# Optimization experiments

Hardware: AMD Instinct MI355X
Metric: run time of the kernel (lower is better)

## Reference

```python
import jax, jax.numpy as jnp
import numpy as np

N_EMBED = 1024
N_HEAD = 16
HEAD_DIM = N_EMBED // N_HEAD


def setup_inputs() -> dict:
    key = jax.random.key(0)
    k1, k2, k3, k4, k5 = jax.random.split(key, 5)
    x = jax.random.normal(k1, (4, 2048, N_EMBED), dtype=jnp.float32)
    s = 1.0 / np.sqrt(N_EMBED)
    W_attn = jax.random.normal(k2, (N_EMBED, 3 * N_EMBED), dtype=jnp.float32) * s
    b_attn = jnp.zeros((3 * N_EMBED,), dtype=jnp.float32)
    W_proj = jax.random.normal(k3, (N_EMBED, N_EMBED), dtype=jnp.float32) * s
    b_proj = jnp.zeros((N_EMBED,), dtype=jnp.float32)
    return {"x": x, "W_attn": W_attn, "b_attn": b_attn, "W_proj": W_proj, "b_proj": b_proj}


def reference(x, W_attn, b_attn, W_proj, b_proj):
    B, T, C = x.shape
    qkv = x @ W_attn + b_attn  # [B, T, 3C]
    q, k, v = jnp.split(qkv, 3, axis=2)
    # [B, H, T, D]
    q = q.reshape(B, T, N_HEAD, HEAD_DIM).transpose(0, 2, 1, 3)
    k = k.reshape(B, T, N_HEAD, HEAD_DIM).transpose(0, 2, 1, 3)
    v = v.reshape(B, T, N_HEAD, HEAD_DIM).transpose(0, 2, 1, 3)
    scale = 1.0 / np.sqrt(HEAD_DIM)
    scores = jnp.einsum('bhqd,bhkd->bhqk', q, k) * scale
    causal = jnp.tril(jnp.ones((T, T), dtype=bool))
    scores = jnp.where(causal[None, None], scores, -jnp.inf)
    attn = jax.nn.softmax(scores, axis=-1)
    y = jnp.einsum('bhqk,bhkd->bhqd', attn, v)
    y = y.transpose(0, 2, 1, 3).reshape(B, T, C)
    return y @ W_proj + b_proj
```

## Files before the change

kernel.cpp:

```cpp
#include <hip/hip_runtime.h>

typedef unsigned short u16;
typedef unsigned int u32;
typedef unsigned long long u64;
typedef __attribute__((ext_vector_type(8))) __bf16 b8;
typedef __attribute__((ext_vector_type(4))) float f32x4;

#define T_SEQ 2048
#define NB 4
#define NH 16
#define HD 64
#define CEMB 1024
#define M_ROWS (NB * T_SEQ)
#define Q_PRESCALE 0.18033688011112042f

__device__ __forceinline__ u16 f2bf(float f) {
  union { float f; unsigned int u; } v; v.f = f;
  unsigned int r = v.u + 0x7FFFu + ((v.u >> 16) & 1u);
  return (u16)(r >> 16);
}

__device__ __forceinline__ u32 pk2bf(float a, float b) {
  __bf16 x = (__bf16)a, y = (__bf16)b;
  return (u32)*(u16*)&x | ((u32)*(u16*)&y << 16);
}

__device__ __forceinline__ void gl_lds16(const u16* g, u16* l) {
  __builtin_amdgcn_global_load_lds(
      (const __attribute__((address_space(1))) unsigned int*)g,
      (__attribute__((address_space(3))) unsigned int*)l, 16, 0, 0);
}

#define BARRIER() __builtin_amdgcn_s_barrier()
#define LGKM0() do { asm volatile("s_waitcnt lgkmcnt(0)" ::: "memory"); \
                     __builtin_amdgcn_sched_barrier(0); } while (0)
#define VMCNT4() asm volatile("s_waitcnt vmcnt(4)" ::: "memory")
#define VMCNT2() asm volatile("s_waitcnt vmcnt(2)" ::: "memory")
#define VMCNT0() asm volatile("s_waitcnt vmcnt(0)" ::: "memory")

__global__ void k_convert(const float* __restrict__ in, u16* __restrict__ out, int n4) {
  int i = blockIdx.x * blockDim.x + threadIdx.x;
  int stride = gridDim.x * blockDim.x;
  for (; i < n4; i += stride) {
    float4 v = ((const float4*)in)[i];
    ushort4 o;
    o.x = f2bf(v.x); o.y = f2bf(v.y); o.z = f2bf(v.z); o.w = f2bf(v.w);
    ((ushort4*)out)[i] = o;
  }
}

__global__ __launch_bounds__(256) void k_transpose(const float* __restrict__ W,
                                                   u16* __restrict__ Wt, int K, int N) {
  __shared__ u16 t[64][65];
  int k0 = blockIdx.y * 64, n0 = blockIdx.x * 64;
  int tx = threadIdx.x & 63, ty = threadIdx.x >> 6;
  for (int i = ty; i < 64; i += 4)
    t[i][tx] = f2bf(W[(size_t)(k0 + i) * N + n0 + tx]);
  __syncthreads();
  for (int i = ty; i < 64; i += 4)
    Wt[(size_t)(n0 + i) * K + k0 + tx] = t[tx][i];
}

template <int MODE, int BNU>
__global__ __launch_bounds__(512, 2) void k_gemm8(const u16* __restrict__ A,
                                                  const u16* __restrict__ Bt,
                                                  const float* __restrict__ bias,
                                                  u16* __restrict__ out_bf,
                                                  float* __restrict__ out_f,
                                                  u16* __restrict__ vt,
                                                  int M, int N, int K, int mstripe) {
  __shared__ u16 sA[2][16384];
  __shared__ u16 sB[2][BNU * 4096];
  constexpr int NI = BNU / 2;
  const int tid = threadIdx.x;
  const int lane = tid & 63;
  const int wid = tid >> 6;
  const int wm = wid >> 2;
  const int wn = wid & 3;
  const int fr = lane & 15;
  const int g = lane >> 4;

  const int xcd = blockIdx.x & 7;
  const int idx = blockIdx.x >> 3;
  const int mt = xcd * mstripe + (idx % mstripe);
  const int nt = idx / mstripe;
  const int row0 = mt * 256, col0 = nt * (BNU * 64);
  const int NT = K >> 6;

  const int kswz = ((lane & 7) ^ ((lane >> 3) & 7)) * 8;
  const u16* gA = A + (size_t)(row0 + wid * 8 + (lane >> 3)) * K + kswz;
  const u16* gB = Bt + (size_t)(col0 + wid * 8 + (lane >> 3)) * K + kswz;

#define SGA(buf, T, u) gl_lds16(gA + (size_t)(u) * 64 * K + (size_t)(T) * 64, \
                                &sA[buf][(u) * 4096 + wid * 512])
#define SGB(buf, T, u) gl_lds16(gB + (size_t)(u) * 64 * K + (size_t)(T) * 64, \
                                &sB[buf][(u) * 4096 + wid * 512])
#define RDA(dst, rowe, ks)                                                     \
  { int row_ = (rowe);                                                         \
    dst = *(const b8*)&sA[bufc][row_ * 64 + ((((ks)*4 + g) ^ (row_ & 7)) << 3)]; }
#define RDB(dst, cole, ks)                                                     \
  { int col_ = (cole);                                                         \
    dst = *(const b8*)&sB[bufc][col_ * 64 + ((((ks)*4 + g) ^ (col_ & 7)) << 3)]; }

  f32x4 acc[8][BNU] = {};
  b8 aF[4][2], bF0[NI][2], bF1[NI][2];

#pragma unroll
  for (int u = 0; u < BNU; ++u) SGB(0, 0, u);
  SGA(0, 0, 0); SGA(0, 0, 2);
  SGA(0, 0, 1); SGA(0, 0, 3);
  SGA(1, 1, 0); SGA(1, 1, 2);
  VMCNT4();
  BARRIER();
  __builtin_amdgcn_sched_barrier(0);

#pragma unroll 2
  for (int T = 0; T < NT; ++T) {
    const int bufc = T & 1, bufn = bufc ^ 1;
    const bool st1 = (T + 1 < NT), st2 = (T + 2 < NT);

#pragma unroll
    for (int mi = 0; mi < 4; ++mi)
#pragma unroll
      for (int ks = 0; ks < 2; ++ks) RDA(aF[mi][ks], wm * 128 + mi * 16 + fr, ks);
#pragma unroll
    for (int ni = 0; ni < NI; ++ni)
#pragma unroll
      for (int ks = 0; ks < 2; ++ks) RDB(bF0[ni][ks], wn * (BNU * 16) + ni * 16 + fr, ks);
    if (st1) { SGB(bufn, T + 1, 0); SGB(bufn, T + 1, 1); }
    else VMCNT0();
    BARRIER(); LGKM0();
    __builtin_amdgcn_s_setprio(1);
#pragma unroll
    for (int mi = 0; mi < 4; ++mi)
#pragma unroll
      for (int ni = 0; ni < NI; ++ni)
#pragma unroll
        for (int ks = 0; ks < 2; ++ks)
          acc[mi][ni] = __builtin_amdgcn_mfma_f32_16x16x32_bf16(aF[mi][ks], bF0[ni][ks], acc[mi][ni], 0, 0, 0);
    __builtin_amdgcn_s_setprio(0);
    __builtin_amdgcn_sched_barrier(0);
    BARRIER();

#pragma unroll
    for (int ni = 0; ni < NI; ++ni)
#pragma unroll
      for (int ks = 0; ks < 2; ++ks) RDB(bF1[ni][ks], wn * (BNU * 16) + (NI + ni) * 16 + fr, ks);
    if (BNU == 4 && st1) { SGB(bufn, T + 1, 2); SGB(bufn, T + 1, 3); }
    if constexpr (BNU == 4) { VMCNT4(); } else { VMCNT2(); }
    BARRIER(); LGKM0();
    __builtin_amdgcn_s_setprio(1);
#pragma unroll
    for (int mi = 0; mi < 4; ++mi)
#pragma unroll
      for (int ni = 0; ni < NI; ++ni)
#pragma unroll
        for (int ks = 0; ks < 2; ++ks)
          acc[mi][NI + ni] = __builtin_amdgcn_mfma_f32_16x16x32_bf16(aF[mi][ks], bF1[ni][ks], acc[mi][NI + ni], 0, 0, 0);
    __builtin_amdgcn_s_setprio(0);
    __builtin_amdgcn_sched_barrier(0);
    BARRIER();

#pragma unroll
    for (int mi = 0; mi < 4; ++mi)
#pragma unroll
      for (int ks = 0; ks < 2; ++ks) RDA(aF[mi][ks], wm * 128 + 64 + mi * 16 + fr, ks);
    if (st2) { SGA(bufc, T + 2, 0); SGA(bufc, T + 2, 2); }
    BARRIER(); LGKM0();
    __builtin_amdgcn_s_setprio(1);
#pragma unroll
    for (int mi = 0; mi < 4; ++mi)
#pragma unroll
      for (int ni = 0; ni < NI; ++ni)
#pragma unroll
        for (int ks = 0; ks < 2; ++ks)
          acc[4 + mi][ni] = __builtin_amdgcn_mfma_f32_16x16x32_bf16(aF[mi][ks], bF0[ni][ks], acc[4 + mi][ni], 0, 0, 0);
    __builtin_amdgcn_s_setprio(0);
    __builtin_amdgcn_sched_barrier(0);
    BARRIER();

    if (st1) { SGA(bufn, T + 1, 1); SGA(bufn, T + 1, 3); }
    VMCNT4();
    BARRIER();
    __builtin_amdgcn_sched_barrier(0);
    __builtin_amdgcn_s_setprio(1);
#pragma unroll
    for (int mi = 0; mi < 4; ++mi)
#pragma unroll
      for (int ni = 0; ni < NI; ++ni)
#pragma unroll
        for (int ks = 0; ks < 2; ++ks)
          acc[4 + mi][NI + ni] = __builtin_amdgcn_mfma_f32_16x16x32_bf16(aF[mi][ks], bF1[ni][ks], acc[4 + mi][NI + ni], 0, 0, 0);
    __builtin_amdgcn_s_setprio(0);
    __builtin_amdgcn_sched_barrier(0);
    BARRIER();
  }
#undef SGA
#undef SGB
#undef RDA
#undef RDB

  const int fg = lane >> 4;
  if (MODE != 2) {
#pragma unroll
    for (int ni = 0; ni < BNU; ++ni) {
      int col = col0 + wn * (BNU * 16) + ni * 16 + fr;
      float bv = bias[col];
#pragma unroll
      for (int mi = 0; mi < 8; ++mi) {
#pragma unroll
        for (int r = 0; r < 4; ++r) {
          int row = row0 + wm * 128 + mi * 16 + fg * 4 + r;
          float v = acc[mi][ni][r] + bv;
          if (MODE == 0) {
            float sc = (col < CEMB) ? Q_PRESCALE : 1.0f;
            out_bf[(size_t)row * (2 * CEMB) + col] = f2bf(v * sc);
          } else {
            out_f[(size_t)row * N + col] = v;
          }
        }
      }
    }
  } else {
    u16* st = (u16*)sA;
    const int bq = row0 >> 11;
    const int t0g = row0 & (T_SEQ - 1);
#pragma unroll
    for (int pass = 0; pass < 2; ++pass) {
      __syncthreads();
      if ((wn >> 1) == pass) {
#pragma unroll
        for (int nn = 0; nn < BNU; ++nn) {
          const int hdl = (wn & 1) * 32 + nn * 16 + fr;
          const float bv = bias[col0 + pass * 64 + hdl];
#pragma unroll
          for (int mi = 0; mi < 8; ++mi) {
            const int tl = wm * 128 + mi * 16 + fg * 4;
#pragma unroll
            for (int rp = 0; rp < 2; ++rp) {
              u32 pk = pk2bf(acc[mi][nn][2 * rp] + bv, acc[mi][nn][2 * rp + 1] + bv);
              *(u32*)&st[hdl * 280 + tl + 2 * rp] = pk;
            }
          }
        }
      }
      __syncthreads();
      const int hd_r = tid >> 3;
      const int ck = tid & 7;
      u16* vrow = vt + ((size_t)(bq * (NH * HD) + col0 + pass * 64 + hd_r)) * T_SEQ + t0g;
#pragma unroll
      for (int j = 0; j < 4; ++j) {
        const int chunk = ck + 8 * j;
        f32x4 d = *(const f32x4*)&st[hd_r * 280 + chunk * 8];
        *(f32x4*)&vrow[chunk * 8] = d;
      }
    }
  }
}

__global__ __launch_bounds__(256) void k_attn(const u16* __restrict__ qk,
                                              const u16* __restrict__ vtg,
                                              u16* __restrict__ y) {
  __shared__ __align__(16) u16 kt_s[2][64 * 64];
  __shared__ __align__(16) u16 vt_s[2][64 * 64];
  __shared__ __align__(16) char pl_s[4][2048];

  const int lane = threadIdx.x & 63;
  const int wave = threadIdx.x >> 6;
  const int tid = threadIdx.x;
  const int g = lane >> 4, c = lane & 15;

  const int orig = blockIdx.x;
  const int xcd = orig & 7;
  const int idx = orig >> 3;
  const int ri = idx >> 3;
  const int hh = idx & 7;
  const int bh = xcd * 8 + hh;
  const int tt = (ri & 4) ? ((ri & 8) ? ri - 12 : ri + 4) : (15 - ri);
  const int b = bh >> 4, h = bh & 15;
  const int qA = tt * 128 + wave * 16;
  const int qB = qA + 64;

  char* plw = pl_s[wave];
  char* plA = plw + c * 128;
  const int b3 = c >> 3;
  const int e2 = (c & 7) << 1;
  const int sb = g + b3 * 8;

  const u16* qrowA = qk + (size_t)(b * T_SEQ + qA + c) * (2 * CEMB) + h * HD + g * 8;
  const b8 qfA0 = *(const b8*)qrowA;
  const b8 qfA1 = *(const b8*)(qrowA + 32);
  const u16* qrowB = qrowA + (size_t)64 * (2 * CEMB);
  const b8 qfB0 = *(const b8*)qrowB;
  const b8 qfB1 = *(const b8*)(qrowB + 32);

  b8 ones_frag;
#pragma unroll
  for (int e = 0; e < 8; ++e) ones_frag[e] = (c == 0) ? (__bf16)1.0f : (__bf16)0.0f;

  const int srow = tid >> 3;
  const int scc = (tid & 7) ^ (srow & 7);
  const u16* ksrc0 = qk + ((size_t)(b * T_SEQ) + srow) * (2 * CEMB) + CEMB + h * HD + scc * 8;
  const u16* vsrc0 = vtg + ((size_t)(bh * HD) + srow) * T_SEQ + scc * 8;

  float mA = -3e38f, mB = -3e38f;
  f32x4 oA[4] = {}, oB[4] = {};
  f32x4 o4A = {0.f, 0.f, 0.f, 0.f}, o4B = {0.f, 0.f, 0.f, 0.f};

  const int nt_tiles = 2 * tt + 2;

#define STAGE(t, bb)                                                    \
  {                                                                     \
    const u16* ks_ = ksrc0 + (size_t)(t) * 64 * (2 * CEMB);             \
    const u16* vs_ = vsrc0 + (t) * 64;                                  \
    gl_lds16(ks_, &kt_s[bb][wave * 512]);                               \
    gl_lds16(ks_ + 32 * (2 * CEMB), &kt_s[bb][wave * 512 + 2048]);      \
    gl_lds16(vs_, &vt_s[bb][wave * 512]);                               \
    gl_lds16(vs_ + 32 * T_SEQ, &vt_s[bb][wave * 512 + 2048]);           \
  }

  STAGE(0, 0);
  __syncthreads();

  int cur = 0;
  for (int t = 0; t < nt_tiles; ++t) {
    if (t + 1 < nt_tiles) STAGE(t + 1, cur ^ 1);
    const int k0 = t * 64;
    const bool lastt = (t == nt_tiles - 1);
    const bool sndl = (t == nt_tiles - 2);
    const u16* kt = kt_s[cur];
    const u16* vtl = vt_s[cur];

    f32x4 sA[4] = {{0.f,0.f,0.f,0.f},{0.f,0.f,0.f,0.f},{0.f,0.f,0.f,0.f},{0.f,0.f,0.f,0.f}};
    f32x4 sB[4] = {{0.f,0.f,0.f,0.f},{0.f,0.f,0.f,0.f},{0.f,0.f,0.f,0.f},{0.f,0.f,0.f,0.f}};
    __builtin_amdgcn_s_setprio(1);
#pragma unroll
    for (int n = 0; n < 4; ++n) {
      const bool needA = (!lastt) && (!sndl || n <= wave);
      const bool needB = (!lastt) || (n <= wave);
      if (needA || needB) {
        const b8 kf0 = *(const b8*)&kt[(n * 16 + c) * 64 + ((g ^ (c & 7)) << 3)];
        const b8 kf1 = *(const b8*)&kt[(n * 16 + c) * 64 + (((4 + g) ^ (c & 7)) << 3)];
        if (needA) {
          sA[n] = __builtin_amdgcn_mfma_f32_16x16x32_bf16(kf0, qfA0, sA[n], 0, 0, 0);
          sA[n] = __builtin_amdgcn_mfma_f32_16x16x32_bf16(kf1, qfA1, sA[n], 0, 0, 0);
        }
        if (needB) {
          sB[n] = __builtin_amdgcn_mfma_f32_16x16x32_bf16(kf0, qfB0, sB[n], 0, 0, 0);
          sB[n] = __builtin_amdgcn_mfma_f32_16x16x32_bf16(kf1, qfB1, sB[n], 0, 0, 0);
        }
      }
    }
    __builtin_amdgcn_s_setprio(0);

    if (sndl) {
#pragma unroll
      for (int n = 0; n < 4; ++n)
#pragma unroll
        for (int r = 0; r < 4; ++r)
          if (k0 + n * 16 + g * 4 + r > qA + c) sA[n][r] = -3e38f;
    }
    if (lastt) {
#pragma unroll
      for (int n = 0; n < 4; ++n)
#pragma unroll
        for (int r = 0; r < 4; ++r)
          if (k0 + n * 16 + g * 4 + r > qB + c) sB[n][r] = -3e38f;
    }

    float rmA = -3e38f, rmB = -3e38f;
    if (!lastt) {
#pragma unroll
      for (int n = 0; n < 4; ++n)
#pragma unroll
        for (int r = 0; r < 4; ++r) rmA = fmaxf(rmA, sA[n][r]);
      rmA = fmaxf(rmA, __shfl_xor(rmA, 16));
      rmA = fmaxf(rmA, __shfl_xor(rmA, 32));
    }
#pragma unroll
    for (int n = 0; n < 4; ++n)
#pragma unroll
      for (int r = 0; r < 4; ++r) rmB = fmaxf(rmB, sB[n][r]);
    rmB = fmaxf(rmB, __shfl_xor(rmB, 16));
    rmB = fmaxf(rmB, __shfl_xor(rmB, 32));

    bool ok = (lastt || rmA <= mA + 8.0f) && (rmB <= mB + 8.0f);
    if (!__all(ok)) {
      float alA = 1.0f, alB;
      if (!lastt) {
        float mn = fmaxf(mA, rmA);
        alA = __builtin_amdgcn_exp2f(mA - mn);
        mA = mn;
      }
      {
        float mn = fmaxf(mB, rmB);
        alB = __builtin_amdgcn_exp2f(mB - mn);
        mB = mn;
      }
#pragma unroll
      for (int r = 0; r < 4; ++r) {
        int src = (lane & 48) + g * 4 + r;
        float aA = __shfl(alA, src);
        float aB = __shfl(alB, src);
#pragma unroll
        for (int nt = 0; nt < 4; ++nt) { oA[nt][r] *= aA; oB[nt][r] *= aB; }
        o4A[r] *= aA; o4B[r] *= aB;
      }
    }

    if (!lastt) {
#pragma unroll
      for (int n = 0; n < 4; ++n) {
        u32 lo = pk2bf(__builtin_amdgcn_exp2f(sA[n][0] - mA),
                       __builtin_amdgcn_exp2f(sA[n][1] - mA));
        u32 hi = pk2bf(__builtin_amdgcn_exp2f(sA[n][2] - mA),
                       __builtin_amdgcn_exp2f(sA[n][3] - mA));
        *(u64*)(plA + ((((4 * n + sb) & 15) ^ e2) << 3)) = ((u64)hi << 32) | lo;
      }
    }
    u64 pbB[4];
#pragma unroll
    for (int n = 0; n < 4; ++n) {
      u32 lo = pk2bf(__builtin_amdgcn_exp2f(sB[n][0] - mB),
                     __builtin_amdgcn_exp2f(sB[n][1] - mB));
      u32 hi = pk2bf(__builtin_amdgcn_exp2f(sB[n][2] - mB),
                     __builtin_amdgcn_exp2f(sB[n][3] - mB));
      pbB[n] = ((u64)hi << 32) | lo;
    }

    b8 vb[2][4];
#pragma unroll
    for (int ks = 0; ks < 2; ++ks)
#pragma unroll
      for (int nt = 0; nt < 4; ++nt)
        vb[ks][nt] = *(const b8*)&vtl[(nt * 16 + c) * 64 + (((ks * 4 + g) ^ (c & 7)) << 3)];

    asm volatile("s_waitcnt lgkmcnt(0)" ::: "memory");
    __builtin_amdgcn_sched_barrier(0);

    if (!lastt) {
      __builtin_amdgcn_s_setprio(1);
#pragma unroll
      for (int ks = 0; ks < 2; ++ks) {
        const b8 paA = *(const b8*)(plA + ((((ks * 8 + 2 * g + 8 * b3) & 15) ^ e2) << 3));
        o4A = __builtin_amdgcn_mfma_f32_16x16x32_bf16(paA, ones_frag, o4A, 0, 0, 0);
#pragma unroll
        for (int nt = 0; nt < 4; ++nt)
          oA[nt] = __builtin_amdgcn_mfma_f32_16x16x32_bf16(paA, vb[ks][nt], oA[nt], 0, 0, 0);
      }
      __builtin_amdgcn_s_setprio(0);
    }

#pragma unroll
    for (int n = 0; n < 4; ++n)
      *(u64*)(plA + ((((4 * n + sb) & 15) ^ e2) << 3)) = pbB[n];
    asm volatile("s_waitcnt lgkmcnt(0)" ::: "memory");
    __builtin_amdgcn_sched_barrier(0);

    __builtin_amdgcn_s_setprio(1);
#pragma unroll
    for (int ks = 0; ks < 2; ++ks) {
      const b8 paB = *(const b8*)(plA + ((((ks * 8 + 2 * g + 8 * b3) & 15) ^ e2) << 3));
      o4B = __builtin_amdgcn_mfma_f32_16x16x32_bf16(paB, ones_frag, o4B, 0, 0, 0);
#pragma unroll
      for (int nt = 0; nt < 4; ++nt)
        oB[nt] = __builtin_amdgcn_mfma_f32_16x16x32_bf16(paB, vb[ks][nt], oB[nt], 0, 0, 0);
    }
    __builtin_amdgcn_s_setprio(0);

    __syncthreads();
    cur ^= 1;
  }
#undef STAGE

#pragma unroll
  for (int r = 0; r < 4; ++r) {
    float lA = __shfl(o4A[r], lane & 48);
    float lB = __shfl(o4B[r], lane & 48);
    float invA = 1.0f / lA;
    float invB = 1.0f / lB;
#pragma unroll
    for (int nt = 0; nt < 4; ++nt) {
      __bf16 va = (__bf16)(oA[nt][r] * invA);
      __bf16 vbv = (__bf16)(oB[nt][r] * invB);
      y[(size_t)(b * T_SEQ + qA + g * 4 + r) * CEMB + h * HD + nt * 16 + c] = *(u16*)&va;
      y[(size_t)(b * T_SEQ + qB + g * 4 + r) * CEMB + h * HD + nt * 16 + c] = *(u16*)&vbv;
    }
  }
}

extern "C" void kernel_launch(void* const* d_in, const int* in_sizes, int n_in,
                              void* d_out, int out_size, void* d_ws, size_t ws_size,
                              hipStream_t stream) {
  const float* x = (const float*)d_in[0];
  const float* W_attn = (const float*)d_in[1];
  const float* b_attn = (const float*)d_in[2];
  const float* W_proj = (const float*)d_in[3];
  const float* b_proj = (const float*)d_in[4];
  float* out = (float*)d_out;

  char* ws = (char*)d_ws;
  u16* x_bf    = (u16*)(ws);
  u16* wattn_t = (u16*)(ws + 16777216);
  u16* wproj_t = (u16*)(ws + 23068672);
  u16* qk_bf   = (u16*)(ws + 25165824);
  u16* vt      = (u16*)(ws + 58720256);
  u16* y_bf    = (u16*)(ws + 75497472);

  k_convert<<<2048, 256, 0, stream>>>(x, x_bf, (NB * T_SEQ * CEMB) / 4);
  k_transpose<<<dim3(3 * CEMB / 64, CEMB / 64), 256, 0, stream>>>(W_attn, wattn_t, CEMB, 3 * CEMB);
  k_transpose<<<dim3(CEMB / 64, CEMB / 64), 256, 0, stream>>>(W_proj, wproj_t, CEMB, CEMB);
  k_gemm8<0, 4><<<256, 512, 0, stream>>>(x_bf, wattn_t, b_attn, qk_bf, nullptr, nullptr,
                                         M_ROWS, 2 * CEMB, CEMB, 4);
  k_gemm8<2, 2><<<256, 512, 0, stream>>>(x_bf, wattn_t + 2048 * CEMB, b_attn + 2 * CEMB,
                                         nullptr, nullptr, vt, M_ROWS, CEMB, CEMB, 4);
  k_attn<<<1024, 256, 0, stream>>>(qk_bf, vt, y_bf);
  k_gemm8<1, 2><<<256, 512, 0, stream>>>(y_bf, wproj_t, b_proj, nullptr, out, nullptr,
                                         M_ROWS, CEMB, CEMB, 4);
}
```

Before: 193.3 us.

## Shrink attention blocks to two waves with paired causal segments per block

The attention kernel now uses 128-thread blocks with 32-row K/V tiles, and each block processes two 64-row query tiles (tt = 31-pr and pr) in sequence, pairing a long and a short causal segment. This replaces the previous 128-query-row tiles with a static remap ordering and is meant to balance causal work across blocks and raise occupancy through smaller LDS and register footprints. In exchange it doubles the number of key tiles and barriers per query row, and each K/V tile is reused by fewer query rows.

```diff
diff --git a/kernel.cpp b/kernel.cpp
--- a/kernel.cpp
+++ b/kernel.cpp
@@ -258,235 +258,226 @@
   }
 }
 
-__global__ __launch_bounds__(256) void k_attn(const u16* __restrict__ qk,
-                                              const u16* __restrict__ vtg,
-                                              u16* __restrict__ y) {
-  __shared__ __align__(16) u16 kt_s[2][64 * 64];
-  __shared__ __align__(16) u16 vt_s[2][64 * 64];
-  __shared__ __align__(16) char pl_s[4][2048];
-
-  const int lane = threadIdx.x & 63;
-  const int wave = threadIdx.x >> 6;
+__global__ __launch_bounds__(128, 4) void k_attn(const u16* __restrict__ qk,
+                                                 const u16* __restrict__ vtg,
+                                                 u16* __restrict__ y) {
+  __shared__ __align__(16) u16 kt_s[2][32 * 64];
+  __shared__ __align__(16) u16 vt_s[2][64 * 32];
+  __shared__ __align__(16) char pl_s[2][1024];
+
   const int tid = threadIdx.x;
+  const int lane = tid & 63;
+  const int w = tid >> 6;
   const int g = lane >> 4, c = lane & 15;
 
-  const int orig = blockIdx.x;
-  const int xcd = orig & 7;
-  const int idx = orig >> 3;
-  const int ri = idx >> 3;
-  const int hh = idx & 7;
-  const int bh = xcd * 8 + hh;
-  const int tt = (ri & 4) ? ((ri & 8) ? ri - 12 : ri + 4) : (15 - ri);
+  const int xcd = blockIdx.x & 7;
+  const int idx = blockIdx.x >> 3;
+  const int bh = xcd * 8 + (idx & 7);
+  const int pr = idx >> 3;
   const int b = bh >> 4, h = bh & 15;
-  const int qA = tt * 128 + wave * 16;
-  const int qB = qA + 64;
-
-  char* plw = pl_s[wave];
-  char* plA = plw + c * 128;
-  const int b3 = c >> 3;
-  const int e2 = (c & 7) << 1;
-  const int sb = g + b3 * 8;
-
-  const u16* qrowA = qk + (size_t)(b * T_SEQ + qA + c) * (2 * CEMB) + h * HD + g * 8;
-  const b8 qfA0 = *(const b8*)qrowA;
-  const b8 qfA1 = *(const b8*)(qrowA + 32);
-  const u16* qrowB = qrowA + (size_t)64 * (2 * CEMB);
-  const b8 qfB0 = *(const b8*)qrowB;
-  const b8 qfB1 = *(const b8*)(qrowB + 32);
+
+  char* plw = pl_s[w];
+  char* plA = plw + c * 64;
+  const int pswz = ((c >> 1) & 3) << 1;
 
   b8 ones_frag;
 #pragma unroll
   for (int e = 0; e < 8; ++e) ones_frag[e] = (c == 0) ? (__bf16)1.0f : (__bf16)0.0f;
 
   const int srow = tid >> 3;
-  const int scc = (tid & 7) ^ (srow & 7);
-  const u16* ksrc0 = qk + ((size_t)(b * T_SEQ) + srow) * (2 * CEMB) + CEMB + h * HD + scc * 8;
-  const u16* vsrc0 = vtg + ((size_t)(bh * HD) + srow) * T_SEQ + scc * 8;
-
-  float mA = -3e38f, mB = -3e38f;
-  f32x4 oA[4] = {}, oB[4] = {};
-  f32x4 o4A = {0.f, 0.f, 0.f, 0.f}, o4B = {0.f, 0.f, 0.f, 0.f};
-
-  const int nt_tiles = 2 * tt + 2;
-
-#define STAGE(t, bb)                                                    \
-  {                                                                     \
-    const u16* ks_ = ksrc0 + (size_t)(t) * 64 * (2 * CEMB);             \
-    const u16* vs_ = vsrc0 + (t) * 64;                                  \
-    gl_lds16(ks_, &kt_s[bb][wave * 512]);                               \
-    gl_lds16(ks_ + 32 * (2 * CEMB), &kt_s[bb][wave * 512 + 2048]);      \
-    gl_lds16(vs_, &vt_s[bb][wave * 512]);                               \
-    gl_lds16(vs_ + 32 * T_SEQ, &vt_s[bb][wave * 512 + 2048]);           \
+  const int kch = (tid & 7) ^ (srow & 7);
+  const u16* ksrc0 = qk + ((size_t)(b * T_SEQ) + srow) * (2 * CEMB) + CEMB + h * HD + kch * 8;
+  const int vdrow = tid >> 2;
+  const int vch = (tid & 3) ^ ((tid >> 3) & 3);
+  const u16* vsrc0 = vtg + ((size_t)(bh * HD) + vdrow) * T_SEQ + vch * 8;
+
+#define STAGE(t, bb)                                                   \
+  {                                                                    \
+    const u16* ks_ = ksrc0 + (size_t)(t) * 32 * (2 * CEMB);            \
+    const u16* vs_ = vsrc0 + (t) * 32;                                 \
+    gl_lds16(ks_, &kt_s[bb][w * 512]);                                 \
+    gl_lds16(ks_ + 16 * (2 * CEMB), &kt_s[bb][1024 + w * 512]);        \
+    gl_lds16(vs_, &vt_s[bb][w * 512]);                                 \
+    gl_lds16(vs_ + 32 * T_SEQ, &vt_s[bb][1024 + w * 512]);             \
   }
 
-  STAGE(0, 0);
-  __syncthreads();
-
   int cur = 0;
-  for (int t = 0; t < nt_tiles; ++t) {
-    if (t + 1 < nt_tiles) STAGE(t + 1, cur ^ 1);
-    const int k0 = t * 64;
-    const bool lastt = (t == nt_tiles - 1);
-    const bool sndl = (t == nt_tiles - 2);
-    const u16* kt = kt_s[cur];
-    const u16* vtl = vt_s[cur];
-
-    f32x4 sA[4] = {{0.f,0.f,0.f,0.f},{0.f,0.f,0.f,0.f},{0.f,0.f,0.f,0.f},{0.f,0.f,0.f,0.f}};
-    f32x4 sB[4] = {{0.f,0.f,0.f,0.f},{0.f,0.f,0.f,0.f},{0.f,0.f,0.f,0.f},{0.f,0.f,0.f,0.f}};
-    __builtin_amdgcn_s_setprio(1);
-#pragma unroll
-    for (int n = 0; n < 4; ++n) {
-      const bool needA = (!lastt) && (!sndl || n <= wave);
-      const bool needB = (!lastt) || (n <= wave);
-      if (needA || needB) {
-        const b8 kf0 = *(const b8*)&kt[(n * 16 + c) * 64 + ((g ^ (c & 7)) << 3)];
-        const b8 kf1 = *(const b8*)&kt[(n * 16 + c) * 64 + (((4 + g) ^ (c & 7)) << 3)];
-        if (needA) {
-          sA[n] = __builtin_amdgcn_mfma_f32_16x16x32_bf16(kf0, qfA0, sA[n], 0, 0, 0);
-          sA[n] = __builtin_amdgcn_mfma_f32_16x16x32_bf16(kf1, qfA1, sA[n], 0, 0, 0);
-        }
-        if (needB) {
-          sB[n] = __builtin_amdgcn_mfma_f32_16x16x32_bf16(kf0, qfB0, sB[n], 0, 0, 0);
-          sB[n] = __builtin_amdgcn_mfma_f32_16x16x32_bf16(kf1, qfB1, sB[n], 0, 0, 0);
-        }
-      }
+#pragma unroll 1
+  for (int seg = 0; seg < 2; ++seg) {
+    const int tt = seg ? pr : (31 - pr);
+    const int q0 = tt * 64;
+    const int qA = q0 + w * 16;
+    const int qB = q0 + 32 + w * 16;
+
+    const u16* qrowA = qk + (size_t)(b * T_SEQ + qA + c) * (2 * CEMB) + h * HD + g * 8;
+    const b8 qfA0 = *(const b8*)qrowA;
+    const b8 qfA1 = *(const b8*)(qrowA + 32);
+    const u16* qrowB = qrowA + (size_t)32 * (2 * CEMB);
+    const b8 qfB0 = *(const b8*)qrowB;
+    const b8 qfB1 = *(const b8*)(qrowB + 32);
+
+    float mA = -3e38f, mB = -3e38f;
+    f32x4 oA[4] = {}, oB[4] = {};
+    f32x4 o4A = {0.f, 0.f, 0.f, 0.f}, o4B = {0.f, 0.f, 0.f, 0.f};
+
+    const int ntt = 2 * tt + 2;
+    STAGE(0, cur);
+    __syncthreads();
+
+    for (int t = 0; t < ntt; ++t) {
+      if (t + 1 < ntt) STAGE(t + 1, cur ^ 1);
+      const bool lastt = (t == ntt - 1);
+      const bool sndl = (t == ntt - 2);
+      const u16* kt = kt_s[cur];
+      const u16* vtl = vt_s[cur];
+
+      f32x4 sA[2] = {{0.f,0.f,0.f,0.f},{0.f,0.f,0.f,0.f}};
+      f32x4 sB[2] = {{0.f,0.f,0.f,0.f},{0.f,0.f,0.f,0.f}};
+      __builtin_amdgcn_s_setprio(1);
+#pragma unroll
+      for (int n = 0; n < 2; ++n) {
+        const bool needA = (!lastt) && (!sndl || n <= w);
+        const bool needB = (!lastt) || (n <= w);
+        if (needA || needB) {
+          const b8 kf0 = *(const b8*)&kt[(n * 16 + c) * 64 + ((g ^ (c & 7)) << 3)];
+          const b8 kf1 = *(const b8*)&kt[(n * 16 + c) * 64 + (((4 + g) ^ (c & 7)) << 3)];
+          if (needA) {
+            sA[n] = __builtin_amdgcn_mfma_f32_16x16x32_bf16(kf0, qfA0, sA[n], 0, 0, 0);
+            sA[n] = __builtin_amdgcn_mfma_f32_16x16x32_bf16(kf1, qfA1, sA[n], 0, 0, 0);
+          }
+          if (needB) {
+            sB[n] = __builtin_amdgcn_mfma_f32_16x16x32_bf16(kf0, qfB0, sB[n], 0, 0, 0);
+            sB[n] = __builtin_amdgcn_mfma_f32_16x16x32_bf16(kf1, qfB1, sB[n], 0, 0, 0);
+          }
+        }
+      }
+      __builtin_amdgcn_s_setprio(0);
+
+      if (sndl) {
+#pragma unroll
+        for (int n = 0; n < 2; ++n)
+#pragma unroll
+          for (int r = 0; r < 4; ++r)
+            if (n * 16 + g * 4 + r > w * 16 + c) sA[n][r] = -3e38f;
+      }
+      if (lastt) {
+#pragma unroll
+        for (int n = 0; n < 2; ++n)
+#pragma unroll
+          for (int r = 0; r < 4; ++r)
+            if (n * 16 + g * 4 + r > w * 16 + c) sB[n][r] = -3e38f;
+      }
+
+      float rmA = -3e38f;
+      if (!lastt) {
+        rmA = fmaxf(fmaxf(fmaxf(sA[0][0], sA[0][1]), fmaxf(sA[0][2], sA[0][3])),
+                    fmaxf(fmaxf(sA[1][0], sA[1][1]), fmaxf(sA[1][2], sA[1][3])));
+        rmA = fmaxf(rmA, __shfl_xor(rmA, 16));
+        rmA = fmaxf(rmA, __shfl_xor(rmA, 32));
+      }
+      float rmB = fmaxf(fmaxf(fmaxf(sB[0][0], sB[0][1]), fmaxf(sB[0][2], sB[0][3])),
+                        fmaxf(fmaxf(sB[1][0], sB[1][1]), fmaxf(sB[1][2], sB[1][3])));
+      rmB = fmaxf(rmB, __shfl_xor(rmB, 16));
+      rmB = fmaxf(rmB, __shfl_xor(rmB, 32));
+
+      bool ok = (lastt || rmA <= mA + 8.0f) && (rmB <= mB + 8.0f);
+      if (!__all(ok)) {
+        float alA = 1.0f, alB;
+        if (!lastt) {
+          float mn = fmaxf(mA, rmA);
+          alA = __builtin_amdgcn_exp2f(mA - mn);
+          mA = mn;
+        }
+        {
+          float mn = fmaxf(mB, rmB);
+          alB = __builtin_amdgcn_exp2f(mB - mn);
+          mB = mn;
+        }
+#pragma unroll
+        for (int r = 0; r < 4; ++r) {
+          int src = (lane & 48) + g * 4 + r;
+          float aA = __shfl(alA, src);
+          float aB = __shfl(alB, src);
+#pragma unroll
+          for (int nt = 0; nt < 4; ++nt) { oA[nt][r] *= aA; oB[nt][r] *= aB; }
+          o4A[r] *= aA; o4B[r] *= aB;
+        }
+      }
+
+      if (!lastt) {
+#pragma unroll
+        for (int n = 0; n < 2; ++n) {
+          u32 lo = pk2bf(__builtin_amdgcn_exp2f(sA[n][0] - mA),
+                         __builtin_amdgcn_exp2f(sA[n][1] - mA));
+          u32 hi = pk2bf(__builtin_amdgcn_exp2f(sA[n][2] - mA),
+                         __builtin_amdgcn_exp2f(sA[n][3] - mA));
+          *(u64*)(plA + (((4 * n + g) ^ pswz) << 3)) = ((u64)hi << 32) | lo;
+        }
+      }
+      u64 pbB[2];
+#pragma unroll
+      for (int n = 0; n < 2; ++n) {
+        u32 lo = pk2bf(__builtin_amdgcn_exp2f(sB[n][0] - mB),
+                       __builtin_amdgcn_exp2f(sB[n][1] - mB));
+        u32 hi = pk2bf(__builtin_amdgcn_exp2f(sB[n][2] - mB),
+                       __builtin_amdgcn_exp2f(sB[n][3] - mB));
+        pbB[n] = ((u64)hi << 32) | lo;
+      }
+
+      b8 vb[4];
+#pragma unroll
+      for (int nt = 0; nt < 4; ++nt)
+        vb[nt] = *(const b8*)&vtl[(nt * 16 + c) * 32 + ((g ^ ((c >> 1) & 3)) << 3)];
+
+      asm volatile("s_waitcnt lgkmcnt(0)" ::: "memory");
+      __builtin_amdgcn_sched_barrier(0);
+
+      if (!lastt) {
+        __builtin_amdgcn_s_setprio(1);
+        const b8 paA = *(const b8*)(plA + (((2 * g) ^ pswz) << 3));
+        o4A = __builtin_amdgcn_mfma_f32_16x16x32_bf16(paA, ones_frag, o4A, 0, 0, 0);
+#pragma unroll
+        for (int nt = 0; nt < 4; ++nt)
+          oA[nt] = __builtin_amdgcn_mfma_f32_16x16x32_bf16(paA, vb[nt], oA[nt], 0, 0, 0);
+        __builtin_amdgcn_s_setprio(0);
+      }
+
+#pragma unroll
+      for (int n = 0; n < 2; ++n)
+        *(u64*)(plA + (((4 * n + g) ^ pswz) << 3)) = pbB[n];
+      asm volatile("s_waitcnt lgkmcnt(0)" ::: "memory");
+      __builtin_amdgcn_sched_barrier(0);
+
+      __builtin_amdgcn_s_setprio(1);
+      {
+        const b8 paB = *(const b8*)(plA + (((2 * g) ^ pswz) << 3));
+        o4B = __builtin_amdgcn_mfma_f32_16x16x32_bf16(paB, ones_frag, o4B, 0, 0, 0);
+#pragma unroll
+        for (int nt = 0; nt < 4; ++nt)
+          oB[nt] = __builtin_amdgcn_mfma_f32_16x16x32_bf16(paB, vb[nt], oB[nt], 0, 0, 0);
+      }
+      __builtin_amdgcn_s_setprio(0);
+
+      __syncthreads();
+      cur ^= 1;
     }
-    __builtin_amdgcn_s_setprio(0);
-
-    if (sndl) {
-#pragma unroll
-      for (int n = 0; n < 4; ++n)
-#pragma unroll
-        for (int r = 0; r < 4; ++r)
-          if (k0 + n * 16 + g * 4 + r > qA + c) sA[n][r] = -3e38f;
+
+#pragma unroll
+    for (int r = 0; r < 4; ++r) {
+      float lA = __shfl(o4A[r], lane & 48);
+      float lB = __shfl(o4B[r], lane & 48);
+      float invA = 1.0f / lA;
+      float invB = 1.0f / lB;
+#pragma unroll
+      for (int nt = 0; nt < 4; ++nt) {
+        __bf16 va = (__bf16)(oA[nt][r] * invA);
+        __bf16 vbv = (__bf16)(oB[nt][r] * invB);
+        y[(size_t)(b * T_SEQ + qA + g * 4 + r) * CEMB + h * HD + nt * 16 + c] = *(u16*)&va;
+        y[(size_t)(b * T_SEQ + qB + g * 4 + r) * CEMB + h * HD + nt * 16 + c] = *(u16*)&vbv;
+      }
     }
-    if (lastt) {
-#pragma unroll
-      for (int n = 0; n < 4; ++n)
-#pragma unroll
-        for (int r = 0; r < 4; ++r)
-          if (k0 + n * 16 + g * 4 + r > qB + c) sB[n][r] = -3e38f;
-    }
-
-    float rmA = -3e38f, rmB = -3e38f;
-    if (!lastt) {
-#pragma unroll
-      for (int n = 0; n < 4; ++n)
-#pragma unroll
-        for (int r = 0; r < 4; ++r) rmA = fmaxf(rmA, sA[n][r]);
-      rmA = fmaxf(rmA, __shfl_xor(rmA, 16));
-      rmA = fmaxf(rmA, __shfl_xor(rmA, 32));
-    }
-#pragma unroll
-    for (int n = 0; n < 4; ++n)
-#pragma unroll
-      for (int r = 0; r < 4; ++r) rmB = fmaxf(rmB, sB[n][r]);
-    rmB = fmaxf(rmB, __shfl_xor(rmB, 16));
-    rmB = fmaxf(rmB, __shfl_xor(rmB, 32));
-
-    bool ok = (lastt || rmA <= mA + 8.0f) && (rmB <= mB + 8.0f);
-    if (!__all(ok)) {
-      float alA = 1.0f, alB;
-      if (!lastt) {
-        float mn = fmaxf(mA, rmA);
-        alA = __builtin_amdgcn_exp2f(mA - mn);
-        mA = mn;
-      }
-      {
-        float mn = fmaxf(mB, rmB);
-        alB = __builtin_amdgcn_exp2f(mB - mn);
-        mB = mn;
-      }
-#pragma unroll
-      for (int r = 0; r < 4; ++r) {
-        int src = (lane & 48) + g * 4 + r;
-        float aA = __shfl(alA, src);
-        float aB = __shfl(alB, src);
-#pragma unroll
-        for (int nt = 0; nt < 4; ++nt) { oA[nt][r] *= aA; oB[nt][r] *= aB; }
-        o4A[r] *= aA; o4B[r] *= aB;
-      }
-    }
-
-    if (!lastt) {
-#pragma unroll
-      for (int n = 0; n < 4; ++n) {
-        u32 lo = pk2bf(__builtin_amdgcn_exp2f(sA[n][0] - mA),
-                       __builtin_amdgcn_exp2f(sA[n][1] - mA));
-        u32 hi = pk2bf(__builtin_amdgcn_exp2f(sA[n][2] - mA),
-                       __builtin_amdgcn_exp2f(sA[n][3] - mA));
-        *(u64*)(plA + ((((4 * n + sb) & 15) ^ e2) << 3)) = ((u64)hi << 32) | lo;
-      }
-    }
-    u64 pbB[4];
-#pragma unroll
-    for (int n = 0; n < 4; ++n) {
-      u32 lo = pk2bf(__builtin_amdgcn_exp2f(sB[n][0] - mB),
-                     __builtin_amdgcn_exp2f(sB[n][1] - mB));
-      u32 hi = pk2bf(__builtin_amdgcn_exp2f(sB[n][2] - mB),
-                     __builtin_amdgcn_exp2f(sB[n][3] - mB));
-      pbB[n] = ((u64)hi << 32) | lo;
-    }
-
-    b8 vb[2][4];
-#pragma unroll
-    for (int ks = 0; ks < 2; ++ks)
-#pragma unroll
-      for (int nt = 0; nt < 4; ++nt)
-        vb[ks][nt] = *(const b8*)&vtl[(nt * 16 + c) * 64 + (((ks * 4 + g) ^ (c & 7)) << 3)];
-
-    asm volatile("s_waitcnt lgkmcnt(0)" ::: "memory");
-    __builtin_amdgcn_sched_barrier(0);
-
-    if (!lastt) {
-      __builtin_amdgcn_s_setprio(1);
-#pragma unroll
-      for (int ks = 0; ks < 2; ++ks) {
-        const b8 paA = *(const b8*)(plA + ((((ks * 8 + 2 * g + 8 * b3) & 15) ^ e2) << 3));
-        o4A = __builtin_amdgcn_mfma_f32_16x16x32_bf16(paA, ones_frag, o4A, 0, 0, 0);
-#pragma unroll
-        for (int nt = 0; nt < 4; ++nt)
-          oA[nt] = __builtin_amdgcn_mfma_f32_16x16x32_bf16(paA, vb[ks][nt], oA[nt], 0, 0, 0);
-      }
-      __builtin_amdgcn_s_setprio(0);
-    }
-
-#pragma unroll
-    for (int n = 0; n < 4; ++n)
-      *(u64*)(plA + ((((4 * n + sb) & 15) ^ e2) << 3)) = pbB[n];
-    asm volatile("s_waitcnt lgkmcnt(0)" ::: "memory");
-    __builtin_amdgcn_sched_barrier(0);
-
-    __builtin_amdgcn_s_setprio(1);
-#pragma unroll
-    for (int ks = 0; ks < 2; ++ks) {
-      const b8 paB = *(const b8*)(plA + ((((ks * 8 + 2 * g + 8 * b3) & 15) ^ e2) << 3));
-      o4B = __builtin_amdgcn_mfma_f32_16x16x32_bf16(paB, ones_frag, o4B, 0, 0, 0);
-#pragma unroll
-      for (int nt = 0; nt < 4; ++nt)
-        oB[nt] = __builtin_amdgcn_mfma_f32_16x16x32_bf16(paB, vb[ks][nt], oB[nt], 0, 0, 0);
-    }
-    __builtin_amdgcn_s_setprio(0);
-
-    __syncthreads();
-    cur ^= 1;
   }
 #undef STAGE
-
-#pragma unroll
-  for (int r = 0; r < 4; ++r) {
-    float lA = __shfl(o4A[r], lane & 48);
-    float lB = __shfl(o4B[r], lane & 48);
-    float invA = 1.0f / lA;
-    float invB = 1.0f / lB;
-#pragma unroll
-    for (int nt = 0; nt < 4; ++nt) {
-      __bf16 va = (__bf16)(oA[nt][r] * invA);
-      __bf16 vbv = (__bf16)(oB[nt][r] * invB);
-      y[(size_t)(b * T_SEQ + qA + g * 4 + r) * CEMB + h * HD + nt * 16 + c] = *(u16*)&va;
-      y[(size_t)(b * T_SEQ + qB + g * 4 + r) * CEMB + h * HD + nt * 16 + c] = *(u16*)&vbv;
-    }
-  }
 }
 
 extern "C" void kernel_launch(void* const* d_in, const int* in_sizes, int n_in,
@@ -514,7 +505,7 @@
                                          M_ROWS, 2 * CEMB, CEMB, 4);
   k_gemm8<2, 2><<<256, 512, 0, stream>>>(x_bf, wattn_t + 2048 * CEMB, b_attn + 2 * CEMB,
                                          nullptr, nullptr, vt, M_ROWS, CEMB, CEMB, 4);
-  k_attn<<<1024, 256, 0, stream>>>(qk_bf, vt, y_bf);
+  k_attn<<<1024, 128, 0, stream>>>(qk_bf, vt, y_bf);
   k_gemm8<1, 2><<<256, 512, 0, stream>>>(y_bf, wproj_t, b_proj, nullptr, out, nullptr,
                                          M_ROWS, CEMB, CEMB, 4);
 }
```

Result: slower. 197.4 us (+2.2%).
